# Kernel optimization log

Measured on AMD Instinct MI355X. Metric: run time of the kernel, lower is better.

The kernel has to match this reference:

```python
import jax, jax.numpy as jnp
import numpy as np

V = 50257   # vocab_size
B = 32      # batch
T = 64      # blk_size (max seq len)
E = 256     # n_emb
H = 8       # n_heads
D = E // H  # head_size = 32
L = 8       # n_layers
F = 4 * E   # ffn hidden = 1024
EPS = 1e-5


def setup_inputs() -> dict:
    key = jax.random.key(0)
    ks = jax.random.split(key, 16)
    s = 0.02  # init std, matching _init_weights
    n = lambda k, shape: jax.random.normal(k, shape, dtype=jnp.float32) * s
    return {
        "ip": jax.random.randint(ks[0], (B, T), 0, V),
        "tok_emb": n(ks[1], (V, E)),
        "pos_emb": n(ks[2], (T, E)),
        # per-layer stacked params (leading axis = layer)
        "Wq": n(ks[3], (L, H, E, D)),
        "Wk": n(ks[4], (L, H, E, D)),
        "Wv": n(ks[5], (L, H, E, D)),
        "Wo": n(ks[6], (L, E, E)),
        "bo": jnp.zeros((L, E), jnp.float32),
        "ln1_g": jnp.ones((L, E), jnp.float32),
        "ln1_b": jnp.zeros((L, E), jnp.float32),
        "ln2_g": jnp.ones((L, E), jnp.float32),
        "ln2_b": jnp.zeros((L, E), jnp.float32),
        "W1": n(ks[7], (L, E, F)),
        "b1": jnp.zeros((L, F), jnp.float32),
        "W2": n(ks[8], (L, F, E)),
        "b2": jnp.zeros((L, E), jnp.float32),
        "lnf_g": jnp.ones((E,), jnp.float32),
        "lnf_b": jnp.zeros((E,), jnp.float32),
        "Wlm": n(ks[9], (E, V)),
        "blm": jnp.zeros((V,), jnp.float32),
    }


def _ln(x, g, b):
    m = jnp.mean(x, axis=-1, keepdims=True)
    v = jnp.var(x, axis=-1, keepdims=True)
    return (x - m) * jax.lax.rsqrt(v + EPS) * g + b


def _gpt(ip, tok_emb, pos_emb, Wq, Wk, Wv, Wo, bo, ln1_g, ln1_b, ln2_g, ln2_b,
         W1, b1, W2, b2, lnf_g, lnf_b, Wlm, blm):
    t = ip.shape[1]
    x = tok_emb[ip] + pos_emb[:t]                      # [B,T,E]
    mask = jnp.tril(jnp.ones((t, t), bool))            # causal
    scale = D ** -0.5

    def block(x, p):
        wq, wk, wv, wo, bo_, g1, b1_, g2, b2_, w1, bb1, w2, bb2 = p
        q = jnp.einsum('btc,hcd->bhtd', x, wq)
        k = jnp.einsum('btc,hcd->bhtd', x, wk)
        v = jnp.einsum('btc,hcd->bhtd', x, wv)
        scores = jnp.einsum('bhtd,bhsd->bhts', q, k) * scale
        scores = jnp.where(mask, scores, -jnp.inf)
        wei = jax.nn.softmax(scores, axis=-1)
        att = jnp.einsum('bhts,bhsd->bhtd', wei, v)
        att = att.transpose(0, 2, 1, 3).reshape(x.shape[0], t, E)  # concat heads
        x = _ln(x + (att @ wo + bo_), g1, b1_)          # post-norm residual
        y = jax.nn.relu(x @ w1 + bb1) @ w2 + bb2        # FFN
        x = _ln(x + y, g2, b2_)
        return x, None

    params = (Wq, Wk, Wv, Wo, bo, ln1_g, ln1_b, ln2_g, ln2_b, W1, b1, W2, b2)
    x, _ = jax.lax.scan(block, x, params)
    x = _ln(x, lnf_g, lnf_b)
    return x @ Wlm + blm                                # [B,T,V] logits


def reference(ip, tok_emb, pos_emb, Wq, Wk, Wv, Wo, bo, ln1_g, ln1_b, ln2_g,
              ln2_b, W1, b1, W2, b2, lnf_g, lnf_b, Wlm, blm):
    return _gpt(ip, tok_emb, pos_emb, Wq, Wk, Wv, Wo, bo, ln1_g, ln1_b,
                ln2_g, ln2_b, W1, b1, W2, b2, lnf_g, lnf_b, Wlm, blm)
```

## Files before the change

### kernel.cpp

```cpp
#include <hip/hip_runtime.h>

#define NB 32
#define NT 64
#define NE 256
#define NH 8
#define ND 32
#define NL 8
#define NF 1024
#define NV 50257
#define NVPAD 50304

typedef __bf16 bf16x8 __attribute__((ext_vector_type(8)));
typedef float f32x4 __attribute__((ext_vector_type(4)));

__device__ __forceinline__ float b2f(unsigned short h) {
  union { unsigned int u; float f; } c; c.u = ((unsigned int)h) << 16; return c.f;
}
__device__ __forceinline__ unsigned short f2b(float f) {
  union { float f; unsigned int u; } c; c.f = f;
  unsigned int u = c.u + 0x7FFFu + ((c.u >> 16) & 1u);
  return (unsigned short)(u >> 16);
}
__device__ __forceinline__ float ldf(const void* p, size_t i, int isbf) {
  return isbf ? b2f(((const unsigned short*)p)[i]) : ((const float*)p)[i];
}
__device__ __forceinline__ int get_isbf(const unsigned int* probe) {
  return (probe[0] == 0x3F800000u) ? 0 : 1;
}

__device__ __forceinline__ void gload16(const unsigned short* g, unsigned short* l) {
  __builtin_amdgcn_global_load_lds(
      (const __attribute__((address_space(1))) unsigned int*)g,
      (__attribute__((address_space(3))) unsigned int*)l, 16, 0, 0);
}

__global__ __launch_bounds__(256)
void transpose_weights_k(const void* __restrict__ Wq, const void* __restrict__ Wk,
                         const void* __restrict__ Wv, const void* __restrict__ Wo,
                         const void* __restrict__ W1, const void* __restrict__ W2,
                         const unsigned int* __restrict__ probe,
                         unsigned short* __restrict__ WqkvT, unsigned short* __restrict__ WoT,
                         unsigned short* __restrict__ W1T, unsigned short* __restrict__ W2T)
{
  __shared__ unsigned short tile[32][33];
  const int isbf = get_isbf(probe);
  const int z = blockIdx.z, x = blockIdx.x;
  const void* src; unsigned short* dst; int K, N, k0, n0;
  size_t soff, doff;
  if (x < 192) {
    const int t = x >> 6, r = x & 63, h = r >> 3, ky = r & 7;
    src = (t == 0) ? Wq : ((t == 1) ? Wk : Wv);
    soff = (size_t)z * 65536 + (size_t)h * 8192; K = 256; N = 32; k0 = ky * 32; n0 = 0;
    dst = WqkvT; doff = (size_t)z * 196608 + (size_t)(t * 256 + h * 32) * 256;
  } else if (x < 256) {
    const int r = x - 192, ny = r >> 3, ky = r & 7;
    src = Wo; soff = (size_t)z * 65536; K = 256; N = 256; k0 = ky * 32; n0 = ny * 32;
    dst = WoT; doff = (size_t)z * 65536;
  } else if (x < 512) {
    const int r = x - 256, ny = r >> 3, ky = r & 7;
    src = W1; soff = (size_t)z * 262144; K = 256; N = 1024; k0 = ky * 32; n0 = ny * 32;
    dst = W1T; doff = (size_t)z * 262144;
  } else {
    const int r = x - 512, ky = r >> 3, ny = r & 7;
    src = W2; soff = (size_t)z * 262144; K = 1024; N = 256; k0 = ky * 32; n0 = ny * 32;
    dst = W2T; doff = (size_t)z * 262144;
  }
  const int tx = threadIdx.x, ty = threadIdx.y;
#pragma unroll
  for (int i = 0; i < 4; ++i) {
    const int k = k0 + ty + i * 8, n = n0 + tx;
    tile[ty + i * 8][tx] = f2b(ldf(src, soff + (size_t)k * N + n, isbf));
  }
  __syncthreads();
#pragma unroll
  for (int i = 0; i < 4; ++i) {
    const int n = n0 + ty + i * 8, k = k0 + tx;
    dst[doff + (size_t)n * K + k] = tile[tx][ty + i * 8];
  }
}

__global__ __launch_bounds__(256)
void transpose_k(const void* __restrict__ srcv, unsigned short* __restrict__ dst,
                 const unsigned int* __restrict__ probe, int K, int N)
{
  __shared__ unsigned short tile[32][33];
  const int isbf = get_isbf(probe);
  const int n0 = blockIdx.x * 32, k0 = blockIdx.y * 32;
  const int tx = threadIdx.x, ty = threadIdx.y;
#pragma unroll
  for (int i = 0; i < 4; ++i) {
    const int k = k0 + ty + i * 8, n = n0 + tx;
    if (k < K && n < N)
      tile[ty + i * 8][tx] = f2b(ldf(srcv, (size_t)k * N + n, isbf));
  }
  __syncthreads();
#pragma unroll
  for (int i = 0; i < 4; ++i) {
    const int n = n0 + ty + i * 8, k = k0 + tx;
    if (n < N && k < K) dst[(size_t)n * K + k] = tile[tx][ty + i * 8];
  }
}

__global__ __launch_bounds__(256)
void embed_k(const int* __restrict__ ip, const void* __restrict__ te,
             const void* __restrict__ pe, const unsigned int* __restrict__ probe,
             float* __restrict__ x, unsigned short* __restrict__ xb)
{
  const int isbf = get_isbf(probe);
  const int i = blockIdx.x * 256 + threadIdx.x;
  const int tp = i >> 8, e = i & 255, t = tp & (NT - 1);
  const int id = ip[tp];
  float v = ldf(te, (size_t)id * NE + e, isbf) + ldf(pe, (size_t)t * NE + e, isbf);
  x[i] = v;
  xb[i] = f2b(v);
}

template<int BM, int BN, int BK, int WM, int WN, bool BIAS, bool RELU, int OUTMODE>
__global__ __launch_bounds__(256)
void gemm_bt(const unsigned short* __restrict__ A, const unsigned short* __restrict__ BT,
             const void* __restrict__ bias, int boff, const unsigned int* __restrict__ probe,
             void* __restrict__ Cv, int M, int N, int K, int ldc)
{
  static_assert((BM / WM) * (BN / WN) == 4, "4 waves");
  static_assert(BK == 64, "BK=64");
  __shared__ __align__(16) unsigned short As[BM * BK];
  __shared__ __align__(16) unsigned short Bs[BN * BK];
  const int tid = threadIdx.x;
  const int lane = tid & 63;
  const int wave = tid >> 6;
  const int m0 = blockIdx.y * BM;
  const int n0 = blockIdx.x * BN;
  constexpr int WAVES_N = BN / WN;
  const int wm = (wave / WAVES_N) * WM;
  const int wn = (wave % WAVES_N) * WN;
  constexpr int MT = WM / 16;
  constexpr int NTt = WN / 16;
  f32x4 acc[MT][NTt] = {};

  constexpr int AITERS = (BM * BK) / 2048;
  constexpr int BITERS = (BN * BK) / 2048;
  const int srow = tid >> 3;
  const int scol = (tid & 7) * 8;
  const int lc = lane & 15;
  const int lk = (lane >> 4) * 8;
  const int lr = (lane >> 4) * 4;

  for (int k0 = 0; k0 < K; k0 += BK) {
#pragma unroll
    for (int it = 0; it < AITERS; ++it)
      gload16(A + (size_t)(m0 + it * 32 + srow) * K + (k0 + scol), &As[it * 2048 + wave * 512]);
#pragma unroll
    for (int it = 0; it < BITERS; ++it)
      gload16(BT + (size_t)(n0 + it * 32 + srow) * K + (k0 + scol), &Bs[it * 2048 + wave * 512]);
    __syncthreads();
#pragma unroll
    for (int ks = 0; ks < BK; ks += 32) {
      bf16x8 afr[MT], bfr[NTt];
#pragma unroll
      for (int i = 0; i < MT; ++i)
        afr[i] = *(const bf16x8*)&As[(wm + i * 16 + lc) * BK + ks + lk];
#pragma unroll
      for (int j = 0; j < NTt; ++j)
        bfr[j] = *(const bf16x8*)&Bs[(wn + j * 16 + lc) * BK + ks + lk];
#pragma unroll
      for (int i = 0; i < MT; ++i)
#pragma unroll
        for (int j = 0; j < NTt; ++j)
          acc[i][j] = __builtin_amdgcn_mfma_f32_16x16x32_bf16(afr[i], bfr[j], acc[i][j], 0, 0, 0);
    }
    __syncthreads();
  }

  int isbf = 1;
  if constexpr (BIAS || OUTMODE == 2) isbf = get_isbf(probe);
#pragma unroll
  for (int i = 0; i < MT; ++i) {
#pragma unroll
    for (int j = 0; j < NTt; ++j) {
      const int col = n0 + wn + j * 16 + lc;
      if (col < N) {
        float bv = BIAS ? ldf(bias, (size_t)(boff + col), isbf) : 0.0f;
#pragma unroll
        for (int q = 0; q < 4; ++q) {
          const int row = m0 + wm + i * 16 + lr + q;
          float v = acc[i][j][q] + bv;
          if (RELU) v = fmaxf(v, 0.0f);
          const size_t idx = (size_t)row * ldc + col;
          if (OUTMODE == 1) ((float*)Cv)[idx] = v;
          else if (OUTMODE == 0) ((unsigned short*)Cv)[idx] = f2b(v);
          else { if (isbf) ((unsigned short*)Cv)[idx] = f2b(v); else ((float*)Cv)[idx] = v; }
        }
      }
    }
  }
}

__global__ __launch_bounds__(256)
void gemm_ln_k(const unsigned short* __restrict__ A, const unsigned short* __restrict__ BT,
               const void* __restrict__ bias, int boff,
               const void* __restrict__ g, const void* __restrict__ b, int goff,
               const unsigned int* __restrict__ probe, const float* __restrict__ xres,
               float* __restrict__ xout, unsigned short* __restrict__ xbout, int K)
{
  __shared__ __align__(16) unsigned short As[32 * 64];
  __shared__ __align__(16) unsigned short Bs[256 * 64];
  __shared__ float vbuf[32][257];
  const int isbf = get_isbf(probe);
  const int tid = threadIdx.x, lane = tid & 63, wave = tid >> 6;
  const int m0 = blockIdx.x * 32;
  const int wn = wave * 64;
  const int srow = tid >> 3, scol = (tid & 7) * 8;
  const int lc = lane & 15, lk = (lane >> 4) * 8, lr = (lane >> 4) * 4;
  f32x4 acc[2][4] = {};

  for (int k0 = 0; k0 < K; k0 += 64) {
    gload16(A + (size_t)(m0 + srow) * K + (k0 + scol), &As[wave * 512]);
#pragma unroll
    for (int it = 0; it < 8; ++it)
      gload16(BT + (size_t)(it * 32 + srow) * K + (k0 + scol), &Bs[it * 2048 + wave * 512]);
    __syncthreads();
#pragma unroll
    for (int ks = 0; ks < 64; ks += 32) {
      bf16x8 afr[2], bfr[4];
#pragma unroll
      for (int i = 0; i < 2; ++i)
        afr[i] = *(const bf16x8*)&As[(i * 16 + lc) * 64 + ks + lk];
#pragma unroll
      for (int j = 0; j < 4; ++j)
        bfr[j] = *(const bf16x8*)&Bs[(wn + j * 16 + lc) * 64 + ks + lk];
#pragma unroll
      for (int i = 0; i < 2; ++i)
#pragma unroll
        for (int j = 0; j < 4; ++j)
          acc[i][j] = __builtin_amdgcn_mfma_f32_16x16x32_bf16(afr[i], bfr[j], acc[i][j], 0, 0, 0);
    }
    __syncthreads();
  }

#pragma unroll
  for (int i = 0; i < 2; ++i) {
#pragma unroll
    for (int j = 0; j < 4; ++j) {
      const int col = wn + j * 16 + lc;
      const float bv = ldf(bias, (size_t)(boff + col), isbf);
#pragma unroll
      for (int q = 0; q < 4; ++q) {
        const int row = i * 16 + lr + q;
        vbuf[row][col] = acc[i][j][q] + bv + xres[(size_t)(m0 + row) * NE + col];
      }
    }
  }
  __syncthreads();

  const int row = tid >> 3, lo = tid & 7;
  float s = 0.0f, s2 = 0.0f;
  for (int c = lo; c < 256; c += 8) { const float v = vbuf[row][c]; s += v; s2 += v * v; }
#pragma unroll
  for (int off = 4; off > 0; off >>= 1) { s += __shfl_xor(s, off); s2 += __shfl_xor(s2, off); }
  const float m = s * (1.0f / NE);
  const float var = s2 * (1.0f / NE) - m * m;
  const float r = rsqrtf(var + 1e-5f);
  for (int c = lo; c < 256; c += 8) {
    const float o = (vbuf[row][c] - m) * r * ldf(g, (size_t)(goff + c), isbf)
                    + ldf(b, (size_t)(goff + c), isbf);
    const size_t idx = (size_t)(m0 + row) * NE + c;
    xout[idx] = o;
    xbout[idx] = f2b(o);
  }
}

__global__ __launch_bounds__(256)
void attn_k(const unsigned short* __restrict__ qkv, unsigned short* __restrict__ att)
{
  const int bh = blockIdx.x, b = bh >> 3, h = bh & 7;
  __shared__ float Q[NT][ND], Kc[NT][ND], Vc[NT][ND];
  __shared__ float pm[4][NT], pl[4][NT];
  __shared__ float pacc[4][NT][ND + 1];
  const int tid = threadIdx.x, wv = tid >> 6, l = tid & 63;
  const unsigned short* base = qkv + (size_t)(b * NT) * (3 * NE) + h * ND;
  for (int i = tid; i < NT * ND; i += 256) {
    const int s = i >> 5, d = i & 31;
    const unsigned short* row = base + s * (3 * NE) + d;
    Q[s][d]  = b2f(row[0]);
    Kc[s][d] = b2f(row[NE]);
    Vc[s][d] = b2f(row[2 * NE]);
  }
  __syncthreads();
  const int t = l;
  float q[ND];
#pragma unroll
  for (int d = 0; d < ND; ++d) q[d] = Q[t][d] * 0.17677669529663689f;
  const int s0 = wv * 16;
  const int s1 = min(s0 + 16, t + 1);
  float mx = -1e30f;
  for (int s = s0; s < s1; ++s) {
    const float4* kp = (const float4*)&Kc[s][0];
    float dot = 0.0f;
#pragma unroll
    for (int c = 0; c < 8; ++c) {
      const float4 kv = kp[c];
      dot += q[c*4+0]*kv.x + q[c*4+1]*kv.y + q[c*4+2]*kv.z + q[c*4+3]*kv.w;
    }
    mx = fmaxf(mx, dot);
  }
  float sum = 0.0f;
  float acc[ND] = {};
  for (int s = s0; s < s1; ++s) {
    const float4* kp = (const float4*)&Kc[s][0];
    float dot = 0.0f;
#pragma unroll
    for (int c = 0; c < 8; ++c) {
      const float4 kv = kp[c];
      dot += q[c*4+0]*kv.x + q[c*4+1]*kv.y + q[c*4+2]*kv.z + q[c*4+3]*kv.w;
    }
    const float e = __expf(dot - mx);
    sum += e;
    const float4* vp = (const float4*)&Vc[s][0];
#pragma unroll
    for (int c = 0; c < 8; ++c) {
      const float4 vv = vp[c];
      acc[c*4+0] += e*vv.x; acc[c*4+1] += e*vv.y; acc[c*4+2] += e*vv.z; acc[c*4+3] += e*vv.w;
    }
  }
  pm[wv][t] = mx; pl[wv][t] = sum;
#pragma unroll
  for (int d = 0; d < ND; ++d) pacc[wv][t][d] = acc[d];
  __syncthreads();

  const int mt = tid >> 2, jj = tid & 3;
  float M = -1e30f;
#pragma unroll
  for (int w = 0; w < 4; ++w) M = fmaxf(M, pm[w][mt]);
  float ew[4], L = 0.0f;
#pragma unroll
  for (int w = 0; w < 4; ++w) { ew[w] = __expf(pm[w][mt] - M); L += pl[w][mt] * ew[w]; }
  const float inv = 1.0f / L;
  unsigned short* op = att + (size_t)(b * NT + mt) * NE + h * ND + jj * 8;
#pragma unroll
  for (int dd = 0; dd < 8; ++dd) {
    float o = 0.0f;
#pragma unroll
    for (int w = 0; w < 4; ++w) o += pacc[w][mt][jj * 8 + dd] * ew[w];
    op[dd] = f2b(o * inv);
  }
}

__global__ __launch_bounds__(256)
void lnf_k(const float* __restrict__ xin, const void* __restrict__ gv,
           const void* __restrict__ bv, const unsigned int* __restrict__ probe,
           unsigned short* __restrict__ xout_b)
{
  const int isbf = get_isbf(probe);
  const int tok = blockIdx.x, e = threadIdx.x;
  const float v = xin[tok * NE + e];
  float s = v, s2 = v * v;
#pragma unroll
  for (int off = 32; off > 0; off >>= 1) {
    s  += __shfl_down(s, off);
    s2 += __shfl_down(s2, off);
  }
  __shared__ float red[10];
  const int wv = e >> 6, ln = e & 63;
  if (ln == 0) { red[wv] = s; red[4 + wv] = s2; }
  __syncthreads();
  if (e == 0) {
    const float ts = red[0] + red[1] + red[2] + red[3];
    const float t2 = red[4] + red[5] + red[6] + red[7];
    const float m = ts * (1.0f / NE);
    const float var = t2 * (1.0f / NE) - m * m;
    red[8] = m; red[9] = rsqrtf(var + 1e-5f);
  }
  __syncthreads();
  const float m = red[8], r = red[9];
  const float o = (v - m) * r * ldf(gv, (size_t)e, isbf) + ldf(bv, (size_t)e, isbf);
  xout_b[tok * NE + e] = f2b(o);
}

extern "C" void kernel_launch(void* const* d_in, const int* in_sizes, int n_in,
                              void* d_out, int out_size, void* d_ws, size_t ws_size,
                              hipStream_t stream) {
  const int* ip = (const int*)d_in[0];
  const void* tok_emb = d_in[1];
  const void* pos_emb = d_in[2];
  const void* Wq = d_in[3];
  const void* Wk = d_in[4];
  const void* Wv = d_in[5];
  const void* Wo = d_in[6];
  const void* bo = d_in[7];
  const void* ln1_g = d_in[8];
  const void* ln1_b = d_in[9];
  const void* ln2_g = d_in[10];
  const void* ln2_b = d_in[11];
  const void* W1 = d_in[12];
  const void* b1 = d_in[13];
  const void* W2 = d_in[14];
  const void* b2 = d_in[15];
  const void* lnf_g = d_in[16];
  const void* lnf_b = d_in[17];
  const void* Wlm = d_in[18];
  const void* blm = d_in[19];
  const unsigned int* probe = (const unsigned int*)ln1_g;

  const int M = NB * NT;

  unsigned short* xb   = (unsigned short*)d_ws;
  unsigned short* xf   = xb   + (size_t)M * NE;
  unsigned short* qkv  = xf   + (size_t)M * NE;
  unsigned short* att  = qkv  + (size_t)M * 3 * NE;
  unsigned short* hbuf = att  + (size_t)M * NE;
  float*          x    = (float*)(hbuf + (size_t)M * NF);
  unsigned short* WqkvT = (unsigned short*)(x + (size_t)M * NE);
  unsigned short* WoT  = WqkvT + (size_t)NL * 768 * NE;
  unsigned short* W1T  = WoT   + (size_t)NL * NE * NE;
  unsigned short* W2T  = W1T   + (size_t)NL * NF * NE;
  unsigned short* WlmT = W2T   + (size_t)NL * NE * NF;

  dim3 tb(32, 8, 1);
  transpose_weights_k<<<dim3(768, 1, NL), tb, 0, stream>>>(
      Wq, Wk, Wv, Wo, W1, W2, probe, WqkvT, WoT, W1T, W2T);
  transpose_k<<<dim3((NV + 31) / 32, NE / 32, 1), tb, 0, stream>>>(Wlm, WlmT, probe, NE, NV);

  embed_k<<<dim3(M), dim3(256), 0, stream>>>(ip, tok_emb, pos_emb, probe, x, xb);

  for (int l = 0; l < NL; ++l) {
    gemm_bt<64, 64, 64, 32, 32, false, false, 0><<<dim3(768 / 64, M / 64), dim3(256), 0, stream>>>(
        xb, WqkvT + (size_t)l * 768 * NE, nullptr, 0, probe, qkv, M, 768, NE, 768);
    attn_k<<<dim3(NB * NH), dim3(256), 0, stream>>>(qkv, att);
    gemm_ln_k<<<dim3(M / 32), dim3(256), 0, stream>>>(
        att, WoT + (size_t)l * NE * NE, bo, l * NE, ln1_g, ln1_b, l * NE,
        probe, x, x, xb, NE);
    gemm_bt<64, 64, 64, 32, 32, true, true, 0><<<dim3(NF / 64, M / 64), dim3(256), 0, stream>>>(
        xb, W1T + (size_t)l * NF * NE, b1, l * NF, probe, hbuf, M, NF, NE, NF);
    gemm_ln_k<<<dim3(M / 32), dim3(256), 0, stream>>>(
        hbuf, W2T + (size_t)l * NE * NF, b2, l * NE, ln2_g, ln2_b, l * NE,
        probe, x, x, xb, NF);
  }

  lnf_k<<<dim3(M), dim3(256), 0, stream>>>(x, lnf_g, lnf_b, probe, xf);

  gemm_bt<128, 128, 64, 64, 64, true, false, 2><<<dim3(NVPAD / 128, M / 128), dim3(256), 0, stream>>>(
      xf, WlmT, blm, 0, probe, d_out, M, NV, NE, NV);
}
```

Before: 1.241 ms.

## Fuse QKV projection into attention kernel and shrink gemm_ln row tiles

The QKV projection GEMM is folded into the attention kernel. Each (batch, head) block computes its own Q, K and V slices with MFMA, loading operands straight from global memory, which removes the qkv intermediate buffer and one launch per layer. The fused GEMM+LayerNorm kernel drops LDS staging, reads fragments directly from global memory, and halves the row tile to 16 so twice as many blocks are launched. The cost is that without shared-memory staging the weight data is re-read from global memory or cache by every block.

```diff
diff --git a/kernel.cpp b/kernel.cpp
--- a/kernel.cpp
+++ b/kernel.cpp
@@ -196,96 +196,40 @@
 }
 
 __global__ __launch_bounds__(256)
-void gemm_ln_k(const unsigned short* __restrict__ A, const unsigned short* __restrict__ BT,
-               const void* __restrict__ bias, int boff,
-               const void* __restrict__ g, const void* __restrict__ b, int goff,
-               const unsigned int* __restrict__ probe, const float* __restrict__ xres,
-               float* __restrict__ xout, unsigned short* __restrict__ xbout, int K)
-{
-  __shared__ __align__(16) unsigned short As[32 * 64];
-  __shared__ __align__(16) unsigned short Bs[256 * 64];
-  __shared__ float vbuf[32][257];
-  const int isbf = get_isbf(probe);
-  const int tid = threadIdx.x, lane = tid & 63, wave = tid >> 6;
-  const int m0 = blockIdx.x * 32;
-  const int wn = wave * 64;
-  const int srow = tid >> 3, scol = (tid & 7) * 8;
-  const int lc = lane & 15, lk = (lane >> 4) * 8, lr = (lane >> 4) * 4;
-  f32x4 acc[2][4] = {};
-
-  for (int k0 = 0; k0 < K; k0 += 64) {
-    gload16(A + (size_t)(m0 + srow) * K + (k0 + scol), &As[wave * 512]);
-#pragma unroll
-    for (int it = 0; it < 8; ++it)
-      gload16(BT + (size_t)(it * 32 + srow) * K + (k0 + scol), &Bs[it * 2048 + wave * 512]);
-    __syncthreads();
-#pragma unroll
-    for (int ks = 0; ks < 64; ks += 32) {
-      bf16x8 afr[2], bfr[4];
-#pragma unroll
-      for (int i = 0; i < 2; ++i)
-        afr[i] = *(const bf16x8*)&As[(i * 16 + lc) * 64 + ks + lk];
-#pragma unroll
-      for (int j = 0; j < 4; ++j)
-        bfr[j] = *(const bf16x8*)&Bs[(wn + j * 16 + lc) * 64 + ks + lk];
-#pragma unroll
-      for (int i = 0; i < 2; ++i)
-#pragma unroll
-        for (int j = 0; j < 4; ++j)
-          acc[i][j] = __builtin_amdgcn_mfma_f32_16x16x32_bf16(afr[i], bfr[j], acc[i][j], 0, 0, 0);
-    }
-    __syncthreads();
-  }
-
-#pragma unroll
-  for (int i = 0; i < 2; ++i) {
-#pragma unroll
-    for (int j = 0; j < 4; ++j) {
-      const int col = wn + j * 16 + lc;
-      const float bv = ldf(bias, (size_t)(boff + col), isbf);
-#pragma unroll
-      for (int q = 0; q < 4; ++q) {
-        const int row = i * 16 + lr + q;
-        vbuf[row][col] = acc[i][j][q] + bv + xres[(size_t)(m0 + row) * NE + col];
-      }
-    }
-  }
-  __syncthreads();
-
-  const int row = tid >> 3, lo = tid & 7;
-  float s = 0.0f, s2 = 0.0f;
-  for (int c = lo; c < 256; c += 8) { const float v = vbuf[row][c]; s += v; s2 += v * v; }
-#pragma unroll
-  for (int off = 4; off > 0; off >>= 1) { s += __shfl_xor(s, off); s2 += __shfl_xor(s2, off); }
-  const float m = s * (1.0f / NE);
-  const float var = s2 * (1.0f / NE) - m * m;
-  const float r = rsqrtf(var + 1e-5f);
-  for (int c = lo; c < 256; c += 8) {
-    const float o = (vbuf[row][c] - m) * r * ldf(g, (size_t)(goff + c), isbf)
-                    + ldf(b, (size_t)(goff + c), isbf);
-    const size_t idx = (size_t)(m0 + row) * NE + c;
-    xout[idx] = o;
-    xbout[idx] = f2b(o);
-  }
-}
-
-__global__ __launch_bounds__(256)
-void attn_k(const unsigned short* __restrict__ qkv, unsigned short* __restrict__ att)
-{
-  const int bh = blockIdx.x, b = bh >> 3, h = bh & 7;
+void qkv_attn_k(const unsigned short* __restrict__ xb, const unsigned short* __restrict__ Wl,
+                unsigned short* __restrict__ att)
+{
+  const int bh = blockIdx.x, bb = bh >> 3, h = bh & 7;
   __shared__ float Q[NT][ND], Kc[NT][ND], Vc[NT][ND];
   __shared__ float pm[4][NT], pl[4][NT];
   __shared__ float pacc[4][NT][ND + 1];
   const int tid = threadIdx.x, wv = tid >> 6, l = tid & 63;
-  const unsigned short* base = qkv + (size_t)(b * NT) * (3 * NE) + h * ND;
-  for (int i = tid; i < NT * ND; i += 256) {
-    const int s = i >> 5, d = i & 31;
-    const unsigned short* row = base + s * (3 * NE) + d;
-    Q[s][d]  = b2f(row[0]);
-    Kc[s][d] = b2f(row[NE]);
-    Vc[s][d] = b2f(row[2 * NE]);
-  }
-  __syncthreads();
+  const int lc = l & 15, lk = (l >> 4) * 8, lr = (l >> 4) * 4;
+
+  f32x4 acc6[6] = {};
+  const unsigned short* Arow = xb + (size_t)(bb * NT + wv * 16 + lc) * NE + lk;
+  const unsigned short* B0 = Wl + (size_t)(h * ND + lc) * NE + lk;
+#pragma unroll 2
+  for (int k0 = 0; k0 < NE; k0 += 32) {
+    bf16x8 afr = *(const bf16x8*)(Arow + k0);
+#pragma unroll
+    for (int j = 0; j < 6; ++j) {
+      const bf16x8 bfr = *(const bf16x8*)(B0 + (size_t)((j >> 1) * 256 + (j & 1) * 16) * NE + k0);
+      acc6[j] = __builtin_amdgcn_mfma_f32_16x16x32_bf16(afr, bfr, acc6[j], 0, 0, 0);
+    }
+  }
+#pragma unroll
+  for (int j = 0; j < 6; ++j) {
+    float* dst = (j >> 1) == 0 ? &Q[0][0] : ((j >> 1) == 1 ? &Kc[0][0] : &Vc[0][0]);
+    const int col = (j & 1) * 16 + lc;
+#pragma unroll
+    for (int qq = 0; qq < 4; ++qq) {
+      const int row = wv * 16 + lr + qq;
+      dst[row * ND + col] = acc6[j][qq];
+    }
+  }
+  __syncthreads();
+
   const int t = l;
   float q[ND];
 #pragma unroll
@@ -335,13 +279,69 @@
 #pragma unroll
   for (int w = 0; w < 4; ++w) { ew[w] = __expf(pm[w][mt] - M); L += pl[w][mt] * ew[w]; }
   const float inv = 1.0f / L;
-  unsigned short* op = att + (size_t)(b * NT + mt) * NE + h * ND + jj * 8;
+  unsigned short* op = att + (size_t)(bb * NT + mt) * NE + h * ND + jj * 8;
 #pragma unroll
   for (int dd = 0; dd < 8; ++dd) {
     float o = 0.0f;
 #pragma unroll
     for (int w = 0; w < 4; ++w) o += pacc[w][mt][jj * 8 + dd] * ew[w];
     op[dd] = f2b(o * inv);
+  }
+}
+
+__global__ __launch_bounds__(256)
+void gemm_ln_k(const unsigned short* __restrict__ A, const unsigned short* __restrict__ BT,
+               const void* __restrict__ bias, int boff,
+               const void* __restrict__ g, const void* __restrict__ b, int goff,
+               const unsigned int* __restrict__ probe, const float* __restrict__ xres,
+               float* __restrict__ xout, unsigned short* __restrict__ xbout, int K)
+{
+  __shared__ float vbuf[16][257];
+  const int isbf = get_isbf(probe);
+  const int tid = threadIdx.x, lane = tid & 63, wave = tid >> 6;
+  const int m0 = blockIdx.x * 16;
+  const int wn = wave * 64;
+  const int lc = lane & 15, lk = (lane >> 4) * 8, lr = (lane >> 4) * 4;
+  f32x4 acc[4] = {};
+
+  const unsigned short* Arow = A + (size_t)(m0 + lc) * K + lk;
+  const unsigned short* Brow = BT + (size_t)(wn + lc) * K + lk;
+#pragma unroll 4
+  for (int k0 = 0; k0 < K; k0 += 32) {
+    const bf16x8 afr = *(const bf16x8*)(Arow + k0);
+#pragma unroll
+    for (int j = 0; j < 4; ++j) {
+      const bf16x8 bfr = *(const bf16x8*)(Brow + (size_t)j * 16 * K + k0);
+      acc[j] = __builtin_amdgcn_mfma_f32_16x16x32_bf16(afr, bfr, acc[j], 0, 0, 0);
+    }
+  }
+
+#pragma unroll
+  for (int j = 0; j < 4; ++j) {
+    const int col = wn + j * 16 + lc;
+    const float bv = ldf(bias, (size_t)(boff + col), isbf);
+#pragma unroll
+    for (int qq = 0; qq < 4; ++qq) {
+      const int row = lr + qq;
+      vbuf[row][col] = acc[j][qq] + bv + xres[(size_t)(m0 + row) * NE + col];
+    }
+  }
+  __syncthreads();
+
+  const int row = tid >> 4, lo = tid & 15;
+  float s = 0.0f, s2 = 0.0f;
+  for (int c = lo; c < 256; c += 16) { const float v = vbuf[row][c]; s += v; s2 += v * v; }
+#pragma unroll
+  for (int off = 8; off > 0; off >>= 1) { s += __shfl_xor(s, off); s2 += __shfl_xor(s2, off); }
+  const float m = s * (1.0f / NE);
+  const float var = s2 * (1.0f / NE) - m * m;
+  const float r = rsqrtf(var + 1e-5f);
+  for (int c = lo; c < 256; c += 16) {
+    const float o = (vbuf[row][c] - m) * r * ldf(g, (size_t)(goff + c), isbf)
+                    + ldf(b, (size_t)(goff + c), isbf);
+    const size_t idx = (size_t)(m0 + row) * NE + c;
+    xout[idx] = o;
+    xbout[idx] = f2b(o);
   }
 }
 
@@ -405,8 +405,7 @@
 
   unsigned short* xb   = (unsigned short*)d_ws;
   unsigned short* xf   = xb   + (size_t)M * NE;
-  unsigned short* qkv  = xf   + (size_t)M * NE;
-  unsigned short* att  = qkv  + (size_t)M * 3 * NE;
+  unsigned short* att  = xf   + (size_t)M * NE;
   unsigned short* hbuf = att  + (size_t)M * NE;
   float*          x    = (float*)(hbuf + (size_t)M * NF);
   unsigned short* WqkvT = (unsigned short*)(x + (size_t)M * NE);
@@ -423,15 +422,14 @@
   embed_k<<<dim3(M), dim3(256), 0, stream>>>(ip, tok_emb, pos_emb, probe, x, xb);
 
   for (int l = 0; l < NL; ++l) {
-    gemm_bt<64, 64, 64, 32, 32, false, false, 0><<<dim3(768 / 64, M / 64), dim3(256), 0, stream>>>(
-        xb, WqkvT + (size_t)l * 768 * NE, nullptr, 0, probe, qkv, M, 768, NE, 768);
-    attn_k<<<dim3(NB * NH), dim3(256), 0, stream>>>(qkv, att);
-    gemm_ln_k<<<dim3(M / 32), dim3(256), 0, stream>>>(
+    qkv_attn_k<<<dim3(NB * NH), dim3(256), 0, stream>>>(
+        xb, WqkvT + (size_t)l * 768 * NE, att);
+    gemm_ln_k<<<dim3(M / 16), dim3(256), 0, stream>>>(
         att, WoT + (size_t)l * NE * NE, bo, l * NE, ln1_g, ln1_b, l * NE,
         probe, x, x, xb, NE);
     gemm_bt<64, 64, 64, 32, 32, true, true, 0><<<dim3(NF / 64, M / 64), dim3(256), 0, stream>>>(
         xb, W1T + (size_t)l * NF * NE, b1, l * NF, probe, hbuf, M, NF, NE, NF);
-    gemm_ln_k<<<dim3(M / 32), dim3(256), 0, stream>>>(
+    gemm_ln_k<<<dim3(M / 16), dim3(256), 0, stream>>>(
         hbuf, W2T + (size_t)l * NE * NF, b2, l * NE, ln2_g, ln2_b, l * NE,
         probe, x, x, xb, NF);
   }
```

Result: slower. 1.283 ms (+3.3%).

## Fuse each transformer layer into a single per-batch-chunk kernel

Applied to the files above, without the earlier changes.

Replaces the five per-layer launches (QKV GEMM, attention, Wo+LN1, FFN1, FFN2+LN2) with one layer kernel. Each 512-thread block owns 16 query rows of one sequence and recomputes K/V for the preceding rows. It keeps Q/K/V, probabilities, attention output, the FFN hidden state and the residual in shared memory, using MFMA for attention as well. Two bf16 activation buffers are ping-ponged across layers so blocks can read other rows' inputs safely. The aim is to cut launch count and global round-trips for intermediates. The cost is redundant K/V computation, only 128 blocks per launch, and weights streamed straight from global/L2 without shared-memory tiling.

```diff
diff --git a/kernel.cpp b/kernel.cpp
--- a/kernel.cpp
+++ b/kernel.cpp
@@ -195,153 +195,269 @@
   }
 }
 
-__global__ __launch_bounds__(256)
-void gemm_ln_k(const unsigned short* __restrict__ A, const unsigned short* __restrict__ BT,
-               const void* __restrict__ bias, int boff,
-               const void* __restrict__ g, const void* __restrict__ b, int goff,
-               const unsigned int* __restrict__ probe, const float* __restrict__ xres,
-               float* __restrict__ xout, unsigned short* __restrict__ xbout, int K)
+__global__ __launch_bounds__(512)
+void layer_k(const unsigned short* __restrict__ xbin, unsigned short* __restrict__ xbout,
+             float* __restrict__ xg,
+             const unsigned short* __restrict__ Wqkv, const unsigned short* __restrict__ Wo,
+             const unsigned short* __restrict__ W1, const unsigned short* __restrict__ W2,
+             const void* __restrict__ bov, const void* __restrict__ b1v, const void* __restrict__ b2v,
+             const void* __restrict__ g1, const void* __restrict__ be1,
+             const void* __restrict__ g2, const void* __restrict__ be2,
+             const unsigned int* __restrict__ probe,
+             int boffo, int boff1, int boff2, int goff)
 {
-  __shared__ __align__(16) unsigned short As[32 * 64];
-  __shared__ __align__(16) unsigned short Bs[256 * 64];
-  __shared__ float vbuf[32][257];
+  const int i = blockIdx.x, b = blockIdx.y;
+  const int T0 = i * 16, ntK = i + 1;
+  const int tid = threadIdx.x, lane = tid & 63, wave = tid >> 6;
+  const int lc = lane & 15, l4 = lane >> 4, lk = l4 * 8, lr = l4 * 4;
   const int isbf = get_isbf(probe);
-  const int tid = threadIdx.x, lane = tid & 63, wave = tid >> 6;
-  const int m0 = blockIdx.x * 32;
-  const int wn = wave * 64;
-  const int srow = tid >> 3, scol = (tid & 7) * 8;
-  const int lc = lane & 15, lk = (lane >> 4) * 8, lr = (lane >> 4) * 4;
-  f32x4 acc[2][4] = {};
-
-  for (int k0 = 0; k0 < K; k0 += 64) {
-    gload16(A + (size_t)(m0 + srow) * K + (k0 + scol), &As[wave * 512]);
-#pragma unroll
-    for (int it = 0; it < 8; ++it)
-      gload16(BT + (size_t)(it * 32 + srow) * K + (k0 + scol), &Bs[it * 2048 + wave * 512]);
+
+  __shared__ __align__(16) char smem[122880];
+  unsigned short (*Ks)[264]   = (unsigned short(*)[264])(smem);
+  unsigned short (*Vt)[72]    = (unsigned short(*)[72])(smem + 33792);
+  unsigned short (*Qs)[264]   = (unsigned short(*)[264])(smem + 70656);
+  unsigned short (*Ps)[72]    = (unsigned short(*)[72])(smem + 79104);
+  unsigned short (*xbo)[264]  = (unsigned short(*)[264])(smem);
+  unsigned short (*hs)[1032]  = (unsigned short(*)[1032])(smem + 8448);
+  unsigned short (*atts)[264] = (unsigned short(*)[264])(smem + 97536);
+  float (*xs)[264]            = (float(*)[264])(smem + 105984);
+
+  {
+    int* vz = (int*)(smem + 33792);
+    for (int jj = tid; jj < 36864 / 4; jj += 512) vz[jj] = 0;
+  }
+  __syncthreads();
+
+  {
+    f32x4 aKV[4][4] = {};
+    f32x4 aQ[2] = {};
+    const unsigned short* Ab = xbin + ((size_t)(b * 64 + lc)) * NE + lk;
+    const int nKV = wave * 64;
+    const int nQ0 = wave * 32;
+#pragma unroll
+    for (int ks = 0; ks < 8; ++ks) {
+      const int k0 = ks * 32;
+      bf16x8 afr[4];
+#pragma unroll
+      for (int mt = 0; mt < 4; ++mt)
+        if (mt <= i) afr[mt] = *(const bf16x8*)(Ab + (size_t)mt * 16 * NE + k0);
+#pragma unroll
+      for (int nt = 0; nt < 4; ++nt) {
+        const bf16x8 bkv = *(const bf16x8*)(Wqkv + (size_t)(256 + nKV + nt * 16 + lc) * NE + k0 + lk);
+#pragma unroll
+        for (int mt = 0; mt < 4; ++mt)
+          if (mt <= i) aKV[mt][nt] = __builtin_amdgcn_mfma_f32_16x16x32_bf16(afr[mt], bkv, aKV[mt][nt], 0, 0, 0);
+      }
+#pragma unroll
+      for (int nt = 0; nt < 2; ++nt) {
+        const bf16x8 bq = *(const bf16x8*)(Wqkv + (size_t)(nQ0 + nt * 16 + lc) * NE + k0 + lk);
+#pragma unroll
+        for (int mt = 0; mt < 4; ++mt)
+          if (mt == i) aQ[nt] = __builtin_amdgcn_mfma_f32_16x16x32_bf16(afr[mt], bq, aQ[nt], 0, 0, 0);
+      }
+    }
+#pragma unroll
+    for (int mt = 0; mt < 4; ++mt) if (mt <= i) {
+#pragma unroll
+      for (int nt = 0; nt < 4; ++nt) {
+        const int n = nKV + nt * 16 + lc;
+#pragma unroll
+        for (int q = 0; q < 4; ++q) {
+          const int row = mt * 16 + lr + q;
+          const unsigned short hv = f2b(aKV[mt][nt][q]);
+          if (n < 256) Ks[row][n] = hv;
+          else Vt[n - 256][row] = hv;
+        }
+      }
+    }
+#pragma unroll
+    for (int nt = 0; nt < 2; ++nt)
+#pragma unroll
+      for (int q = 0; q < 4; ++q)
+        Qs[lr + q][nQ0 + nt * 16 + lc] = f2b(aQ[nt][q] * 0.17677669529663689f);
+  }
+  __syncthreads();
+
+  {
+    const int h = wave;
+    f32x4 s[4];
+    const bf16x8 qf = *(const bf16x8*)&Qs[lc][h * 32 + lk];
+#pragma unroll
+    for (int nt = 0; nt < 4; ++nt) {
+      if (nt < ntK) {
+        const bf16x8 kf = *(const bf16x8*)&Ks[nt * 16 + lc][h * 32 + lk];
+        f32x4 z = {};
+        s[nt] = __builtin_amdgcn_mfma_f32_16x16x32_bf16(qf, kf, z, 0, 0, 0);
+      }
+    }
+    float mx[4] = {-3e38f, -3e38f, -3e38f, -3e38f};
+#pragma unroll
+    for (int nt = 0; nt < 4; ++nt) if (nt < ntK) {
+#pragma unroll
+      for (int q = 0; q < 4; ++q) {
+        const int key = nt * 16 + lc, qg = T0 + lr + q;
+        float v = s[nt][q];
+        v = (key <= qg) ? v : -1e30f;
+        s[nt][q] = v;
+        mx[q] = fmaxf(mx[q], v);
+      }
+    }
+#pragma unroll
+    for (int off = 8; off; off >>= 1)
+#pragma unroll
+      for (int q = 0; q < 4; ++q) mx[q] = fmaxf(mx[q], __shfl_xor(mx[q], off));
+    float ls[4] = {};
+#pragma unroll
+    for (int nt = 0; nt < 4; ++nt) {
+#pragma unroll
+      for (int q = 0; q < 4; ++q) {
+        float p = 0.0f;
+        if (nt < ntK) { p = __expf(s[nt][q] - mx[q]); ls[q] += p; }
+        Ps[h * 16 + lr + q][nt * 16 + lc] = f2b(p);
+      }
+    }
+#pragma unroll
+    for (int off = 8; off; off >>= 1)
+#pragma unroll
+      for (int q = 0; q < 4; ++q) ls[q] += __shfl_xor(ls[q], off);
+    float inv[4];
+#pragma unroll
+    for (int q = 0; q < 4; ++q) inv[q] = 1.0f / ls[q];
     __syncthreads();
-#pragma unroll
-    for (int ks = 0; ks < 64; ks += 32) {
-      bf16x8 afr[2], bfr[4];
-#pragma unroll
-      for (int i = 0; i < 2; ++i)
-        afr[i] = *(const bf16x8*)&As[(i * 16 + lc) * 64 + ks + lk];
-#pragma unroll
-      for (int j = 0; j < 4; ++j)
-        bfr[j] = *(const bf16x8*)&Bs[(wn + j * 16 + lc) * 64 + ks + lk];
-#pragma unroll
-      for (int i = 0; i < 2; ++i)
-#pragma unroll
-        for (int j = 0; j < 4; ++j)
-          acc[i][j] = __builtin_amdgcn_mfma_f32_16x16x32_bf16(afr[i], bfr[j], acc[i][j], 0, 0, 0);
-    }
-    __syncthreads();
-  }
-
-#pragma unroll
-  for (int i = 0; i < 2; ++i) {
-#pragma unroll
-    for (int j = 0; j < 4; ++j) {
-      const int col = wn + j * 16 + lc;
-      const float bv = ldf(bias, (size_t)(boff + col), isbf);
+    f32x4 o[2] = {};
+#pragma unroll
+    for (int kt = 0; kt < 2; ++kt) {
+      const bf16x8 pf = *(const bf16x8*)&Ps[h * 16 + lc][kt * 32 + lk];
+#pragma unroll
+      for (int dt = 0; dt < 2; ++dt) {
+        const bf16x8 vf = *(const bf16x8*)&Vt[h * 32 + dt * 16 + lc][kt * 32 + lk];
+        o[dt] = __builtin_amdgcn_mfma_f32_16x16x32_bf16(pf, vf, o[dt], 0, 0, 0);
+      }
+    }
+#pragma unroll
+    for (int dt = 0; dt < 2; ++dt)
+#pragma unroll
+      for (int q = 0; q < 4; ++q)
+        atts[lr + q][h * 32 + dt * 16 + lc] = f2b(o[dt][q] * inv[q]);
+  }
+  __syncthreads();
+
+  {
+    f32x4 a2[2] = {};
+    const int nC0 = wave * 32;
+#pragma unroll
+    for (int ks = 0; ks < 8; ++ks) {
+      const int k0 = ks * 32;
+      const bf16x8 af = *(const bf16x8*)&atts[lc][k0 + lk];
+#pragma unroll
+      for (int nt = 0; nt < 2; ++nt) {
+        const bf16x8 bf = *(const bf16x8*)(Wo + (size_t)(nC0 + nt * 16 + lc) * NE + k0 + lk);
+        a2[nt] = __builtin_amdgcn_mfma_f32_16x16x32_bf16(af, bf, a2[nt], 0, 0, 0);
+      }
+    }
+#pragma unroll
+    for (int nt = 0; nt < 2; ++nt) {
+      const int col = nC0 + nt * 16 + lc;
+      const float bv = ldf(bov, (size_t)(boffo + col), isbf);
 #pragma unroll
       for (int q = 0; q < 4; ++q) {
-        const int row = i * 16 + lr + q;
-        vbuf[row][col] = acc[i][j][q] + bv + xres[(size_t)(m0 + row) * NE + col];
-      }
-    }
-  }
-  __syncthreads();
-
-  const int row = tid >> 3, lo = tid & 7;
-  float s = 0.0f, s2 = 0.0f;
-  for (int c = lo; c < 256; c += 8) { const float v = vbuf[row][c]; s += v; s2 += v * v; }
-#pragma unroll
-  for (int off = 4; off > 0; off >>= 1) { s += __shfl_xor(s, off); s2 += __shfl_xor(s2, off); }
-  const float m = s * (1.0f / NE);
-  const float var = s2 * (1.0f / NE) - m * m;
-  const float r = rsqrtf(var + 1e-5f);
-  for (int c = lo; c < 256; c += 8) {
-    const float o = (vbuf[row][c] - m) * r * ldf(g, (size_t)(goff + c), isbf)
-                    + ldf(b, (size_t)(goff + c), isbf);
-    const size_t idx = (size_t)(m0 + row) * NE + c;
-    xout[idx] = o;
-    xbout[idx] = f2b(o);
-  }
-}
-
-__global__ __launch_bounds__(256)
-void attn_k(const unsigned short* __restrict__ qkv, unsigned short* __restrict__ att)
-{
-  const int bh = blockIdx.x, b = bh >> 3, h = bh & 7;
-  __shared__ float Q[NT][ND], Kc[NT][ND], Vc[NT][ND];
-  __shared__ float pm[4][NT], pl[4][NT];
-  __shared__ float pacc[4][NT][ND + 1];
-  const int tid = threadIdx.x, wv = tid >> 6, l = tid & 63;
-  const unsigned short* base = qkv + (size_t)(b * NT) * (3 * NE) + h * ND;
-  for (int i = tid; i < NT * ND; i += 256) {
-    const int s = i >> 5, d = i & 31;
-    const unsigned short* row = base + s * (3 * NE) + d;
-    Q[s][d]  = b2f(row[0]);
-    Kc[s][d] = b2f(row[NE]);
-    Vc[s][d] = b2f(row[2 * NE]);
-  }
-  __syncthreads();
-  const int t = l;
-  float q[ND];
-#pragma unroll
-  for (int d = 0; d < ND; ++d) q[d] = Q[t][d] * 0.17677669529663689f;
-  const int s0 = wv * 16;
-  const int s1 = min(s0 + 16, t + 1);
-  float mx = -1e30f;
-  for (int s = s0; s < s1; ++s) {
-    const float4* kp = (const float4*)&Kc[s][0];
-    float dot = 0.0f;
-#pragma unroll
-    for (int c = 0; c < 8; ++c) {
-      const float4 kv = kp[c];
-      dot += q[c*4+0]*kv.x + q[c*4+1]*kv.y + q[c*4+2]*kv.z + q[c*4+3]*kv.w;
-    }
-    mx = fmaxf(mx, dot);
-  }
-  float sum = 0.0f;
-  float acc[ND] = {};
-  for (int s = s0; s < s1; ++s) {
-    const float4* kp = (const float4*)&Kc[s][0];
-    float dot = 0.0f;
-#pragma unroll
-    for (int c = 0; c < 8; ++c) {
-      const float4 kv = kp[c];
-      dot += q[c*4+0]*kv.x + q[c*4+1]*kv.y + q[c*4+2]*kv.z + q[c*4+3]*kv.w;
-    }
-    const float e = __expf(dot - mx);
-    sum += e;
-    const float4* vp = (const float4*)&Vc[s][0];
-#pragma unroll
-    for (int c = 0; c < 8; ++c) {
-      const float4 vv = vp[c];
-      acc[c*4+0] += e*vv.x; acc[c*4+1] += e*vv.y; acc[c*4+2] += e*vv.z; acc[c*4+3] += e*vv.w;
-    }
-  }
-  pm[wv][t] = mx; pl[wv][t] = sum;
-#pragma unroll
-  for (int d = 0; d < ND; ++d) pacc[wv][t][d] = acc[d];
-  __syncthreads();
-
-  const int mt = tid >> 2, jj = tid & 3;
-  float M = -1e30f;
-#pragma unroll
-  for (int w = 0; w < 4; ++w) M = fmaxf(M, pm[w][mt]);
-  float ew[4], L = 0.0f;
-#pragma unroll
-  for (int w = 0; w < 4; ++w) { ew[w] = __expf(pm[w][mt] - M); L += pl[w][mt] * ew[w]; }
-  const float inv = 1.0f / L;
-  unsigned short* op = att + (size_t)(b * NT + mt) * NE + h * ND + jj * 8;
-#pragma unroll
-  for (int dd = 0; dd < 8; ++dd) {
-    float o = 0.0f;
-#pragma unroll
-    for (int w = 0; w < 4; ++w) o += pacc[w][mt][jj * 8 + dd] * ew[w];
-    op[dd] = f2b(o * inv);
+        const int row = lr + q;
+        xs[row][col] = a2[nt][q] + bv + xg[(size_t)(b * 64 + T0 + row) * NE + col];
+      }
+    }
+  }
+  __syncthreads();
+
+  {
+    const int row = tid >> 5, t5 = tid & 31;
+    float s = 0.0f, s2 = 0.0f;
+#pragma unroll
+    for (int j = 0; j < 8; ++j) { const float v = xs[row][t5 + j * 32]; s += v; s2 += v * v; }
+#pragma unroll
+    for (int off = 16; off; off >>= 1) { s += __shfl_xor(s, off); s2 += __shfl_xor(s2, off); }
+    const float m = s * (1.0f / NE);
+    const float var = s2 * (1.0f / NE) - m * m;
+    const float r = rsqrtf(var + 1e-5f);
+#pragma unroll
+    for (int j = 0; j < 8; ++j) {
+      const int c = t5 + j * 32;
+      const float o = (xs[row][c] - m) * r * ldf(g1, (size_t)(goff + c), isbf)
+                      + ldf(be1, (size_t)(goff + c), isbf);
+      xs[row][c] = o;
+      xbo[row][c] = f2b(o);
+    }
+  }
+  __syncthreads();
+
+  {
+    f32x4 a1[8] = {};
+    const int nD0 = wave * 128;
+#pragma unroll
+    for (int ks = 0; ks < 8; ++ks) {
+      const int k0 = ks * 32;
+      const bf16x8 af = *(const bf16x8*)&xbo[lc][k0 + lk];
+#pragma unroll
+      for (int nt = 0; nt < 8; ++nt) {
+        const bf16x8 bf = *(const bf16x8*)(W1 + (size_t)(nD0 + nt * 16 + lc) * NE + k0 + lk);
+        a1[nt] = __builtin_amdgcn_mfma_f32_16x16x32_bf16(af, bf, a1[nt], 0, 0, 0);
+      }
+    }
+#pragma unroll
+    for (int nt = 0; nt < 8; ++nt) {
+      const int col = nD0 + nt * 16 + lc;
+      const float bv = ldf(b1v, (size_t)(boff1 + col), isbf);
+#pragma unroll
+      for (int q = 0; q < 4; ++q)
+        hs[lr + q][col] = f2b(fmaxf(a1[nt][q] + bv, 0.0f));
+    }
+  }
+  __syncthreads();
+
+  {
+    f32x4 a2[2] = {};
+    const int nE0 = wave * 32;
+#pragma unroll 8
+    for (int ks = 0; ks < 32; ++ks) {
+      const int k0 = ks * 32;
+      const bf16x8 af = *(const bf16x8*)&hs[lc][k0 + lk];
+#pragma unroll
+      for (int nt = 0; nt < 2; ++nt) {
+        const bf16x8 bf = *(const bf16x8*)(W2 + (size_t)(nE0 + nt * 16 + lc) * NF + k0 + lk);
+        a2[nt] = __builtin_amdgcn_mfma_f32_16x16x32_bf16(af, bf, a2[nt], 0, 0, 0);
+      }
+    }
+#pragma unroll
+    for (int nt = 0; nt < 2; ++nt) {
+      const int col = nE0 + nt * 16 + lc;
+      const float bv = ldf(b2v, (size_t)(boff2 + col), isbf);
+#pragma unroll
+      for (int q = 0; q < 4; ++q) {
+        const int row = lr + q;
+        xs[row][col] = a2[nt][q] + bv + xs[row][col];
+      }
+    }
+  }
+  __syncthreads();
+
+  {
+    const int row = tid >> 5, t5 = tid & 31;
+    float s = 0.0f, s2 = 0.0f;
+#pragma unroll
+    for (int j = 0; j < 8; ++j) { const float v = xs[row][t5 + j * 32]; s += v; s2 += v * v; }
+#pragma unroll
+    for (int off = 16; off; off >>= 1) { s += __shfl_xor(s, off); s2 += __shfl_xor(s2, off); }
+    const float m = s * (1.0f / NE);
+    const float var = s2 * (1.0f / NE) - m * m;
+    const float r = rsqrtf(var + 1e-5f);
+    const size_t gr = (size_t)(b * 64 + T0 + row) * NE;
+#pragma unroll
+    for (int j = 0; j < 8; ++j) {
+      const int c = t5 + j * 32;
+      const float o = (xs[row][c] - m) * r * ldf(g2, (size_t)(goff + c), isbf)
+                      + ldf(be2, (size_t)(goff + c), isbf);
+      xg[gr + c] = o;
+      xbout[gr + c] = f2b(o);
+    }
   }
 }
 
@@ -403,11 +519,10 @@
 
   const int M = NB * NT;
 
-  unsigned short* xb   = (unsigned short*)d_ws;
-  unsigned short* xf   = xb   + (size_t)M * NE;
-  unsigned short* qkv  = xf   + (size_t)M * NE;
-  unsigned short* att  = qkv  + (size_t)M * 3 * NE;
-  unsigned short* hbuf = att  + (size_t)M * NE;
+  unsigned short* xbA  = (unsigned short*)d_ws;
+  unsigned short* xf   = xbA  + (size_t)M * NE;
+  unsigned short* xbB  = xf   + (size_t)M * NE;
+  unsigned short* hbuf = xbB  + (size_t)M * NE;
   float*          x    = (float*)(hbuf + (size_t)M * NF);
   unsigned short* WqkvT = (unsigned short*)(x + (size_t)M * NE);
   unsigned short* WoT  = WqkvT + (size_t)NL * 768 * NE;
@@ -420,20 +535,17 @@
       Wq, Wk, Wv, Wo, W1, W2, probe, WqkvT, WoT, W1T, W2T);
   transpose_k<<<dim3((NV + 31) / 32, NE / 32, 1), tb, 0, stream>>>(Wlm, WlmT, probe, NE, NV);
 
-  embed_k<<<dim3(M), dim3(256), 0, stream>>>(ip, tok_emb, pos_emb, probe, x, xb);
+  embed_k<<<dim3(M), dim3(256), 0, stream>>>(ip, tok_emb, pos_emb, probe, x, xbA);
 
   for (int l = 0; l < NL; ++l) {
-    gemm_bt<64, 64, 64, 32, 32, false, false, 0><<<dim3(768 / 64, M / 64), dim3(256), 0, stream>>>(
-        xb, WqkvT + (size_t)l * 768 * NE, nullptr, 0, probe, qkv, M, 768, NE, 768);
-    attn_k<<<dim3(NB * NH), dim3(256), 0, stream>>>(qkv, att);
-    gemm_ln_k<<<dim3(M / 32), dim3(256), 0, stream>>>(
-        att, WoT + (size_t)l * NE * NE, bo, l * NE, ln1_g, ln1_b, l * NE,
-        probe, x, x, xb, NE);
-    gemm_bt<64, 64, 64, 32, 32, true, true, 0><<<dim3(NF / 64, M / 64), dim3(256), 0, stream>>>(
-        xb, W1T + (size_t)l * NF * NE, b1, l * NF, probe, hbuf, M, NF, NE, NF);
-    gemm_ln_k<<<dim3(M / 32), dim3(256), 0, stream>>>(
-        hbuf, W2T + (size_t)l * NE * NF, b2, l * NE, ln2_g, ln2_b, l * NE,
-        probe, x, x, xb, NF);
+    const unsigned short* xin = (l & 1) ? xbB : xbA;
+    unsigned short* xout      = (l & 1) ? xbA : xbB;
+    layer_k<<<dim3(4, NB), dim3(512), 0, stream>>>(
+        xin, xout, x,
+        WqkvT + (size_t)l * 768 * NE, WoT + (size_t)l * NE * NE,
+        W1T + (size_t)l * NF * NE, W2T + (size_t)l * NE * NF,
+        bo, b1, b2, ln1_g, ln1_b, ln2_g, ln2_b, probe,
+        l * NE, l * NF, l * NE, l * NE);
   }
 
   lnf_k<<<dim3(M), dim3(256), 0, stream>>>(x, lnf_g, lnf_b, probe, xf);
```

Measured after the change: 1.195 ms. 3.7% less time.
